# Kernel tuning notes

Hardware: AMD Instinct MI355X
Metric: run time of the kernel (lower is better)

Reference implementation:

```python
import jax, jax.numpy as jnp
import numpy as np

K_NN = 20  # neighbors per group (k=20 in source)


def fps_one(xyz, npoint):
    # xyz: [N,3] -> indices [npoint] via iterative furthest point sampling
    N = xyz.shape[0]
    def body(carry, _):
        dist, far = carry
        d = jnp.sum((xyz - xyz[far]) ** 2, axis=-1)
        dist = jnp.minimum(dist, d)
        return (dist, jnp.argmax(dist).astype(jnp.int32)), far
    init = (jnp.full((N,), 1e10, xyz.dtype), jnp.int32(0))
    _, idx = jax.lax.scan(body, init, None, length=npoint)
    return idx


def gather(pts, idx):
    # pts: [B,M,C], idx: [B,...] -> [B,...,C]
    return jax.vmap(lambda p, i: p[i])(pts, idx)


def knn(q, ref, k):
    # q: [B,S,3], ref: [B,M,3] -> [B,S,k] indices of nearest refs
    d = (jnp.sum(q * q, -1, keepdims=True)
         - 2.0 * jnp.einsum('bsc,bmc->bsm', q, ref)
         + jnp.sum(ref * ref, -1)[:, None, :])
    _, idx = jax.lax.top_k(-d, k)
    return idx


def sa_block(xyz, feats, npoint, W, b):
    # Set abstraction: FPS sample -> kNN group -> shared MLP -> max pool
    fidx = jax.vmap(fps_one, in_axes=(0, None))(xyz, npoint)   # [B,S]
    new_xyz = gather(xyz, fidx)                                 # [B,S,3]
    nidx = knn(new_xyz, xyz, K_NN)                              # [B,S,K]
    rel = gather(xyz, nidx) - new_xyz[:, :, None, :]            # [B,S,K,3]
    grp = jnp.concatenate([rel, gather(feats, nidx)], -1)       # [B,S,K,3+C]
    h = jax.nn.relu(jnp.einsum('bskc,cd->bskd', grp, W) + b)
    return new_xyz, jnp.max(h, axis=2)                          # [B,S,Cout]


def fp_block(xq, xr, fr, skip, W, b):
    # Feature propagation: 3-NN inverse-distance interp -> concat skip -> MLP
    idx = knn(xq, xr, 3)                                        # [B,S,3]
    d = jnp.sum((gather(xr, idx) - xq[:, :, None, :]) ** 2, -1)
    w = 1.0 / (d + 1e-8)
    w = w / jnp.sum(w, -1, keepdims=True)
    interp = jnp.einsum('bsk,bskc->bsc', w, gather(fr, idx))
    cat = jnp.concatenate([interp, skip], -1)
    return jax.nn.relu(jnp.einsum('bsc,cd->bsd', cat, W) + b)


def setup_inputs() -> dict:
    key = jax.random.key(0)
    ks = jax.random.split(key, 24)
    B, N = 8, 4096
    x = jax.random.normal(ks[0], (B, 6, N), jnp.float32)
    cls_label = jax.random.uniform(ks[1], (B, 16), jnp.float32)
    def lin(k, cin, cout):
        kw, kb = jax.random.split(k)
        s = 1.0 / np.sqrt(cin)
        return (jax.random.normal(kw, (cin, cout), jnp.float32) * s,
                jax.random.normal(kb, (cout,), jnp.float32) * 0.01)
    W0, b0 = lin(ks[2], 6, 64)
    W1, b1 = lin(ks[3], 67, 128)
    W2, b2 = lin(ks[4], 131, 256)
    W3, b3 = lin(ks[5], 259, 512)
    F3, fb3 = lin(ks[6], 768, 512)
    F2, fb2 = lin(ks[7], 640, 256)
    F1, fb1 = lin(ks[8], 320, 128)
    F0, fb0 = lin(ks[9], 150, 128)
    Wseg, bseg = lin(ks[10], 128, 50)
    return {"x": x, "cls_label": cls_label,
            "W0": W0, "b0": b0, "W1": W1, "b1": b1, "W2": W2, "b2": b2,
            "W3": W3, "b3": b3, "F3": F3, "fb3": fb3, "F2": F2, "fb2": fb2,
            "F1": F1, "fb1": fb1, "F0": F0, "fb0": fb0,
            "Wseg": Wseg, "bseg": bseg}


def reference(x, cls_label, W0, b0, W1, b1, W2, b2, W3, b3,
              F3, fb3, F2, fb2, F1, fb1, F0, fb0, Wseg, bseg):
    B, _, N = x.shape
    xyz = jnp.transpose(x[:, :3, :], (0, 2, 1))   # [B,N,3]
    nrm = jnp.transpose(x[:, 3:, :], (0, 2, 1))   # [B,N,3]
    # hierarchical set abstraction (512 -> 256 -> 128 -> 64 points)
    x1, f1 = sa_block(xyz, nrm, 512, W0, b0)      # f1: [B,512,64]
    x2, f2 = sa_block(x1, f1, 256, W1, b1)        # f2: [B,256,128]
    x3, f3 = sa_block(x2, f2, 128, W2, b2)        # f3: [B,128,256]
    x4, f4 = sa_block(x3, f3, 64, W3, b3)         # f4: [B,64,512]
    # feature propagation back up
    g3 = fp_block(x3, x4, f4, f3, F3, fb3)        # [B,128,512]
    g2 = fp_block(x2, x3, g3, f2, F2, fb2)        # [B,256,256]
    g1 = fp_block(x1, x2, g2, f1, F1, fb1)        # [B,512,128]
    cls = jnp.broadcast_to(cls_label[:, None, :], (B, N, 16))
    skip0 = jnp.concatenate([cls, xyz, nrm], -1)  # [B,N,22]
    g0 = fp_block(xyz, x1, g1, skip0, F0, fb0)    # [B,N,128]
    result = jnp.einsum('bnc,cd->bnd', g0, Wseg) + bseg  # [B,N,50]
    return result, jnp.transpose(g0, (0, 2, 1))
```

## Files before the change

kernel.cpp:

```cpp
#include <hip/hip_runtime.h>
#include <float.h>

#define B8 8
#define NPTS 4096

template <int CTRL, int RM>
__device__ __forceinline__ unsigned dppmov(unsigned v) {
  return (unsigned)__builtin_amdgcn_update_dpp((int)v, (int)v, CTRL, RM, 0xf, false);
}

template <int CTRL, int RM>
__device__ __forceinline__ void red_key_max(unsigned& kh, unsigned& kl) {
  unsigned oh = dppmov<CTRL, RM>(kh);
  unsigned ol = dppmov<CTRL, RM>(kl);
  unsigned long long ko = ((unsigned long long)oh << 32) | ol;
  unsigned long long k  = ((unsigned long long)kh << 32) | kl;
  bool c = ko > k;
  kh = c ? oh : kh;
  kl = c ? ol : kl;
}

template <int CTRL, int RM>
__device__ __forceinline__ void red_key_min(unsigned& kh, unsigned& kl) {
  unsigned oh = dppmov<CTRL, RM>(kh);
  unsigned ol = dppmov<CTRL, RM>(kl);
  unsigned long long ko = ((unsigned long long)oh << 32) | ol;
  unsigned long long k  = ((unsigned long long)kh << 32) | kl;
  bool c = ko < k;
  kh = c ? oh : kh;
  kl = c ? ol : kl;
}

#define WAVE_RED_MAX(kh, kl)            \
  red_key_max<0x111, 0xf>(kh, kl);      \
  red_key_max<0x112, 0xf>(kh, kl);      \
  red_key_max<0x114, 0xf>(kh, kl);      \
  red_key_max<0x118, 0xf>(kh, kl);      \
  red_key_max<0x142, 0xa>(kh, kl);      \
  red_key_max<0x143, 0xc>(kh, kl);

#define WAVE_RED_MIN(kh, kl)            \
  red_key_min<0x111, 0xf>(kh, kl);      \
  red_key_min<0x112, 0xf>(kh, kl);      \
  red_key_min<0x114, 0xf>(kh, kl);      \
  red_key_min<0x118, 0xf>(kh, kl);      \
  red_key_min<0x142, 0xa>(kh, kl);      \
  red_key_min<0x143, 0xc>(kh, kl);

template <int BLOCK, int P>
__global__ __launch_bounds__(BLOCK) void fps4_kernel(const float* __restrict__ x,
                                                     float* __restrict__ xyz,
                                                     float* __restrict__ nrm,
                                                     float4* __restrict__ xyz4,
                                                     int N, int S,
                                                     float* __restrict__ out_xyz) {
#pragma clang fp contract(off)
  constexpr int NW = BLOCK / 64;
  __shared__ float4 pts[BLOCK * P];
  __shared__ float4 sel[512];
  __shared__ alignas(16) unsigned long long wkey[2][NW];
  int b = blockIdx.x, t = threadIdx.x;
  const float* xb = x + (size_t)b * 6 * N;
  float px[P], py[P], pz[P], dist[P];
#pragma unroll
  for (int j = 0; j < P; ++j) {
    int idx = t + j * BLOCK;
    float a = xb[0 * N + idx], bb = xb[1 * N + idx], c = xb[2 * N + idx];
    px[j] = a; py[j] = bb; pz[j] = c;
    pts[idx] = make_float4(a, bb, c, 0.f);
    dist[j] = 1e10f;
    size_t g = (size_t)b * N + idx;
    float* o1 = xyz + g * 3;
    o1[0] = a; o1[1] = bb; o1[2] = c;
    xyz4[g] = make_float4(a, bb, c, a * a + bb * bb + c * c);
    float n0 = xb[3 * N + idx], n1 = xb[4 * N + idx], n2 = xb[5 * N + idx];
    float* o2 = nrm + g * 3;
    o2[0] = n0; o2[1] = n1; o2[2] = n2;
  }
  __syncthreads();
  float fx = xb[0], fy = xb[N], fz = xb[2 * N];
  for (int i = 0; i < S; ++i) {
    if (t == 0) sel[i] = make_float4(fx, fy, fz, 0.f);
    float bv = -1.0f;
    int bj = 0;
#pragma unroll
    for (int j = 0; j < P; ++j) {
      float dx = px[j] - fx, dy = py[j] - fy, dz = pz[j] - fz;
      float d = dx * dx + dy * dy + dz * dz;
      float nd = fminf(dist[j], d);
      dist[j] = nd;
      bool c = nd > bv;
      bv = c ? nd : bv;
      bj = c ? j : bj;
    }
    unsigned kh = __float_as_uint(bv);
    unsigned kl = (unsigned)(~(t + bj * BLOCK));
    WAVE_RED_MAX(kh, kl);
    int buf = i & 1;
    if ((t & 63) == 63)
      wkey[buf][t >> 6] = ((unsigned long long)kh << 32) | kl;
    __syncthreads();
    unsigned long long g = 0ull;
    const ulonglong2* wk2 = (const ulonglong2*)&wkey[buf][0];
#pragma unroll
    for (int w = 0; w < NW / 2; ++w) {
      ulonglong2 e = wk2[w];
      unsigned long long m = (e.x > e.y) ? e.x : e.y;
      g = (m > g) ? m : g;
    }
    int far = (int)~(unsigned)g;
    float4 f = pts[far];
    fx = f.x; fy = f.y; fz = f.z;
  }
  __syncthreads();
  for (int i = t; i < S; i += BLOCK) {
    float4 f = sel[i];
    float* o = out_xyz + ((size_t)b * S + i) * 3;
    o[0] = f.x; o[1] = f.y; o[2] = f.z;
  }
}

__global__ __launch_bounds__(64) void knn20_kernel(const float* __restrict__ q,
                                                   const float4* __restrict__ ref4,
                                                   const float* __restrict__ nrm,
                                                   const float* __restrict__ W,
                                                   const float* __restrict__ bias,
                                                   float* __restrict__ f1) {
#pragma clang fp contract(off)
  int bs = blockIdx.x;
  int b = bs >> 9;
  int t = threadIdx.x;
  __shared__ alignas(16) float smem_in[20][8];
  const float* qp = q + (size_t)bs * 3;
  float qx = qp[0], qy = qp[1], qz = qp[2];
  float qq = qx * qx + qy * qy + qz * qz;
  const float4* rp = ref4 + (size_t)b * 4096;
  float v1 = FLT_MAX, v2 = FLT_MAX;
  int i1 = 0, i2 = 0;
  for (int k = 0; k < 64; ++k) {
    int i = t + (k << 6);
    float4 r = rp[i];
    float dot = qx * r.x + qy * r.y + qz * r.z;
    float d = qq - 2.0f * dot + r.w;
    if (d < v1) { v2 = v1; i2 = i1; v1 = d; i1 = i; }
    else if (d < v2) { v2 = d; i2 = i; }
  }
  unsigned long long taken = 0ull;
  unsigned keep = 0;
  for (int k = 0; k < 20; ++k) {
    unsigned kh = __float_as_uint(v1), kl = (unsigned)i1;
    WAVE_RED_MIN(kh, kl);
    unsigned w = (unsigned)__builtin_amdgcn_readlane((int)kl, 63);
    if (t == k) keep = w;
    if (((int)w & 63) == t) {
      taken |= 1ull << ((int)w >> 6);
      v1 = v2; i1 = i2;
      v2 = FLT_MAX; i2 = 0;
      if (v1 == FLT_MAX) {
        for (int j = 0; j < 64; ++j) {
          if ((taken >> j) & 1ull) continue;
          int i = t + (j << 6);
          float4 r = rp[i];
          float dot = qx * r.x + qy * r.y + qz * r.z;
          float d = qq - 2.0f * dot + r.w;
          if (d < v1) { v2 = v1; i2 = i1; v1 = d; i1 = i; }
          else if (d < v2) { v2 = d; i2 = i; }
        }
      }
    }
  }
  if (t < 20) {
    int id = (int)keep;
    float4 r = rp[id];
    const float* nr = nrm + ((size_t)b * 4096 + id) * 3;
    smem_in[t][0] = r.x - qx;
    smem_in[t][1] = r.y - qy;
    smem_in[t][2] = r.z - qz;
    smem_in[t][3] = nr[0];
    smem_in[t][4] = nr[1];
    smem_in[t][5] = nr[2];
    smem_in[t][6] = 0.0f;
    smem_in[t][7] = 0.0f;
  }
  __syncthreads();
  float w0 = W[0 * 64 + t], w1 = W[1 * 64 + t], w2 = W[2 * 64 + t];
  float w3 = W[3 * 64 + t], w4 = W[4 * 64 + t], w5 = W[5 * 64 + t];
  float bb = bias[t];
  float m = 0.0f;
  for (int n = 0; n < 20; ++n) {
    const float4 a = *reinterpret_cast<const float4*>(&smem_in[n][0]);
    const float4 c = *reinterpret_cast<const float4*>(&smem_in[n][4]);
    float v = a.x * w0;
    v += a.y * w1;
    v += a.z * w2;
    v += a.w * w3;
    v += c.x * w4;
    v += c.y * w5;
    v += bb;
    m = fmaxf(m, v);
  }
  f1[(size_t)bs * 64 + t] = m;
}

__device__ __forceinline__ void knn3_store(int g, const float* rx3,
                                           float qx, float qy, float qz,
                                           int i0, int i1, int i2,
                                           int* __restrict__ idx3,
                                           float* __restrict__ w3) {
#pragma clang fp contract(off)
  int ii[3] = {i0, i1, i2};
  float w[3];
  float wsum = 0.0f;
#pragma unroll
  for (int k = 0; k < 3; ++k) {
    const float* r = rx3 + (size_t)ii[k] * 3;
    float dx = r[0] - qx, dy = r[1] - qy, dz = r[2] - qz;
    float d = dx * dx + dy * dy + dz * dz;
    w[k] = 1.0f / (d + 1e-8f);
    wsum += w[k];
  }
#pragma unroll
  for (int k = 0; k < 3; ++k) {
    idx3[(size_t)g * 3 + k] = ii[k];
    w3[(size_t)g * 3 + k] = w[k] / wsum;
  }
}

__global__ __launch_bounds__(256) void neighbors_kernel(
    const float* __restrict__ xyz, const float* __restrict__ x1,
    int* __restrict__ nidx2, int* __restrict__ nidx3, int* __restrict__ nidx4,
    int* __restrict__ idx3_3, float* __restrict__ w3_3,
    int* __restrict__ idx3_2, float* __restrict__ w3_2,
    int* __restrict__ idx3_1, float* __restrict__ w3_1,
    int* __restrict__ idx3_0, float* __restrict__ w3_0) {
#pragma clang fp contract(off)
  __shared__ float4 smem4[512];
  int blk = blockIdx.x, tid = threadIdx.x;

  if (blk < 896) {
    int S, M, qid;
    int* nout;
    const int wv = tid >> 6, t64 = tid & 63;
    if (blk < 512)      { S = 256; M = 512; qid = blk * 4 + wv;         nout = nidx2; }
    else if (blk < 768) { S = 128; M = 256; qid = (blk - 512) * 4 + wv; nout = nidx3; }
    else                { S = 64;  M = 128; qid = (blk - 768) * 4 + wv; nout = nidx4; }
    float* swd = (float*)smem4 + wv * M;
    int b = qid / S, s = qid % S;
    const float* qp = x1 + ((size_t)b * 512 + s) * 3;
    float qx = qp[0], qy = qp[1], qz = qp[2];
    float qq = qx * qx + qy * qy + qz * qz;
    const float* rp = x1 + (size_t)b * 512 * 3;
    for (int i = t64; i < M; i += 64) {
      float rx = rp[3 * i], ry = rp[3 * i + 1], rz = rp[3 * i + 2];
      float rr = rx * rx + ry * ry + rz * rz;
      float dot = qx * rx + qy * ry + qz * rz;
      swd[i] = qq - 2.0f * dot + rr;
    }
    __syncthreads();
    unsigned keep = 0;
    for (int k = 0; k < 20; ++k) {
      float bv = FLT_MAX;
      int bi = 0;
      for (int i = t64; i < M; i += 64) {
        float v = swd[i];
        bool c = v < bv;
        bv = c ? v : bv;
        bi = c ? i : bi;
      }
      unsigned kh = __float_as_uint(bv), kl = (unsigned)bi;
      WAVE_RED_MIN(kh, kl);
      unsigned w = (unsigned)__builtin_amdgcn_readlane((int)kl, 63);
      if (t64 == k) keep = w;
      if (t64 == 0) swd[w] = FLT_MAX;
      __syncthreads();
    }
    if (t64 < 20) nout[(size_t)qid * 20 + t64] = (int)keep;
    return;
  }

  if (blk < 900) {
    int g = (blk - 896) * 256 + tid;
    int Sq = 128, M = 64;
    int b = g / Sq, s = g % Sq;
    const float* qp = x1 + ((size_t)b * 512 + s) * 3;
    float qx = qp[0], qy = qp[1], qz = qp[2];
    float qq = qx * qx + qy * qy + qz * qz;
    const float* rp = x1 + (size_t)b * 512 * 3;
    float v0 = FLT_MAX, v1 = FLT_MAX, v2 = FLT_MAX;
    int i0 = 0, i1 = 0, i2 = 0;
    for (int i = 0; i < M; ++i) {
      float rx = rp[3 * i], ry = rp[3 * i + 1], rz = rp[3 * i + 2];
      float d = qq - 2.0f * (qx * rx + qy * ry + qz * rz) + (rx * rx + ry * ry + rz * rz);
      if (d < v2) {
        if (d < v1) {
          if (d < v0) { v2 = v1; i2 = i1; v1 = v0; i1 = i0; v0 = d; i0 = i; }
          else { v2 = v1; i2 = i1; v1 = d; i1 = i; }
        } else { v2 = d; i2 = i; }
      }
    }
    knn3_store(g, rp, qx, qy, qz, i0, i1, i2, idx3_3, w3_3);
    return;
  }

  int g, Sq, M, LDQ;
  int* oidx;
  float* ow;
  const float* q;
  if (blk < 908)      { g = (blk - 900) * 256 + tid; Sq = 256;  M = 128; oidx = idx3_2; ow = w3_2; q = x1;  LDQ = 512; }
  else if (blk < 924) { g = (blk - 908) * 256 + tid; Sq = 512;  M = 256; oidx = idx3_1; ow = w3_1; q = x1;  LDQ = 512; }
  else                { g = (blk - 924) * 256 + tid; Sq = 4096; M = 512; oidx = idx3_0; ow = w3_0; q = xyz; LDQ = 4096; }
  int b = g / Sq, s = g % Sq;
  const float* rp = x1 + (size_t)b * 512 * 3;
  for (int i = tid; i < M; i += 256) {
    float rx = rp[3 * i], ry = rp[3 * i + 1], rz = rp[3 * i + 2];
    smem4[i] = make_float4(rx, ry, rz, rx * rx + ry * ry + rz * rz);
  }
  __syncthreads();
  const float* qp = q + ((size_t)b * LDQ + s) * 3;
  float qx = qp[0], qy = qp[1], qz = qp[2];
  float qq = qx * qx + qy * qy + qz * qz;
  float v0 = FLT_MAX, v1 = FLT_MAX, v2 = FLT_MAX;
  int i0 = 0, i1 = 0, i2 = 0;
  for (int i = 0; i < M; ++i) {
    float4 r = smem4[i];
    float d = qq - 2.0f * (qx * r.x + qy * r.y + qz * r.z) + r.w;
    if (d < v2) {
      if (d < v1) {
        if (d < v0) { v2 = v1; i2 = i1; v1 = v0; i1 = i0; v0 = d; i0 = i; }
        else { v2 = v1; i2 = i1; v1 = d; i1 = i; }
      } else { v2 = d; i2 = i; }
    }
  }
  {
    int ii[3] = {i0, i1, i2};
    float w[3];
    float wsum = 0.0f;
#pragma unroll
    for (int k = 0; k < 3; ++k) {
      float4 r = smem4[ii[k]];
      float dx = r.x - qx, dy = r.y - qy, dz = r.z - qz;
      float d = dx * dx + dy * dy + dz * dz;
      w[k] = 1.0f / (d + 1e-8f);
      wsum += w[k];
    }
#pragma unroll
    for (int k = 0; k < 3; ++k) {
      oidx[(size_t)g * 3 + k] = ii[k];
      ow[(size_t)g * 3 + k] = w[k] / wsum;
    }
  }
}

#define GEMM_SHARED                                                               \
  __shared__ alignas(16) float As[2][16][68];                                     \
  __shared__ alignas(16) float Bs[2][16][64];

#define GEMM_STAGE(k0v, ...)                                                      \
    {                                                                             \
      int kq0 = (k0v) + (((int)threadIdx.x >> 6) << 2);                           \
      float4 va = make_float4(0.f, 0.f, 0.f, 0.f);                                \
      { __VA_ARGS__ }                                                             \
      areg4 = va;                                                                 \
    }                                                                             \
    {                                                                             \
      int kk = (int)threadIdx.x >> 4;                                             \
      int n4 = ((int)threadIdx.x & 15) * 4;                                       \
      int kq = (k0v) + kk, cc = colBase + n4;                                     \
      if (colBase + 64 <= N) {                                                    \
        if (kq < K) breg4 = *reinterpret_cast<const float4*>(&Wm[(size_t)kq * N + cc]); \
        else breg4 = make_float4(0.f, 0.f, 0.f, 0.f);                             \
      } else {                                                                    \
        breg4.x = (kq < K && cc < N) ? Wm[(size_t)kq * N + cc] : 0.0f;            \
        breg4.y = (kq < K && cc + 1 < N) ? Wm[(size_t)kq * N + cc + 1] : 0.0f;    \
        breg4.z = (kq < K && cc + 2 < N) ? Wm[(size_t)kq * N + cc + 2] : 0.0f;    \
        breg4.w = (kq < K && cc + 3 < N) ? Wm[(size_t)kq * N + cc + 3] : 0.0f;    \
      }                                                                           \
    }

#define GEMM_WRITE_LDS(bufv)                                                      \
    {                                                                             \
      int r_ = (int)threadIdx.x & 63;                                             \
      int k4_ = ((int)threadIdx.x >> 6) * 4;                                      \
      As[bufv][k4_ + 0][r_] = areg4.x;                                            \
      As[bufv][k4_ + 1][r_] = areg4.y;                                            \
      As[bufv][k4_ + 2][r_] = areg4.z;                                            \
      As[bufv][k4_ + 3][r_] = areg4.w;                                            \
    }                                                                             \
    *reinterpret_cast<float4*>(&Bs[bufv][threadIdx.x >> 4][(threadIdx.x & 15) * 4]) = breg4;

#define GEMM_MAIN(...)                                                            \
  int tx = threadIdx.x & 15, ty = threadIdx.x >> 4;                               \
  float acc[4][4] = {};                                                           \
  float4 areg4, breg4;                                                            \
  GEMM_STAGE(kLo, __VA_ARGS__)                                                    \
  GEMM_WRITE_LDS(0)                                                               \
  __syncthreads();                                                                \
  int cur = 0;                                                                    \
  for (int k0 = kLo; k0 < kHi; k0 += 16) {                                        \
    int nxt = cur ^ 1;                                                            \
    bool more = (k0 + 16 < kHi);                                                  \
    if (more) { GEMM_STAGE(k0 + 16, __VA_ARGS__) }                                \
    _Pragma("unroll")                                                             \
    for (int kk = 0; kk < 16; ++kk) {                                             \
      const float4 av = *reinterpret_cast<const float4*>(&As[cur][kk][ty * 4]);   \
      const float4 bv = *reinterpret_cast<const float4*>(&Bs[cur][kk][tx * 4]);   \
      acc[0][0] += av.x * bv.x; acc[0][1] += av.x * bv.y;                         \
      acc[0][2] += av.x * bv.z; acc[0][3] += av.x * bv.w;                         \
      acc[1][0] += av.y * bv.x; acc[1][1] += av.y * bv.y;                         \
      acc[1][2] += av.y * bv.z; acc[1][3] += av.y * bv.w;                         \
      acc[2][0] += av.z * bv.x; acc[2][1] += av.z * bv.y;                         \
      acc[2][2] += av.z * bv.z; acc[2][3] += av.z * bv.w;                         \
      acc[3][0] += av.w * bv.x; acc[3][1] += av.w * bv.y;                         \
      acc[3][2] += av.w * bv.z; acc[3][3] += av.w * bv.w;                         \
    }                                                                             \
    if (more) { GEMM_WRITE_LDS(nxt) }                                             \
    __syncthreads();                                                              \
    cur = nxt;                                                                    \
  }

#define GEMM_EPI_STORE                                                            \
  _Pragma("unroll")                                                               \
  for (int i = 0; i < 4; ++i) {                                                   \
    int row = rowBase + ty * 4 + i;                                               \
    if (row >= Mrows) continue;                                                   \
    _Pragma("unroll")                                                             \
    for (int j = 0; j < 4; ++j) {                                                 \
      int col = colBase + tx * 4 + j;                                             \
      if (col >= N) continue;                                                     \
      float v = acc[i][j] + bias[col];                                            \
      if (RELU) v = fmaxf(v, 0.0f);                                               \
      C[(size_t)row * N + col] = v;                                               \
    }                                                                             \
  }

__global__ __launch_bounds__(256) void gemm_seg_kernel(const float* __restrict__ A,
                                                       const float* __restrict__ Wm,
                                                       const float* __restrict__ bias,
                                                       float* __restrict__ C,
                                                       float* __restrict__ T,
                                                       int Mrows, int N, int K) {
  GEMM_SHARED
  const int kLo = 0, kHi = K;
  const int RELU = 0;
  int rowBase = blockIdx.y * 64;
  int colBase = blockIdx.x * 64;
  const int rowA = rowBase + ((int)threadIdx.x & 63);
  const float* arow = A + (size_t)rowA * K;
  float* tbase = T + ((size_t)(rowA >> 12) * 128) * 4096 + (rowA & 4095);
  GEMM_MAIN(
    va = *reinterpret_cast<const float4*>(&arow[kq0]);
    {
      float* tp = tbase + (size_t)kq0 * 4096;
      tp[0] = va.x; tp[4096] = va.y; tp[8192] = va.z; tp[12288] = va.w;
    }
  )
  GEMM_EPI_STORE
}

__global__ __launch_bounds__(256) void gemm_sa_kernel(
    const float* __restrict__ xyz, const float* __restrict__ feats,
    const float* __restrict__ new_xyz, const int* __restrict__ nidx,
    const float* __restrict__ Wm, const float* __restrict__ bias,
    float* __restrict__ fOut, int Mref, int LDR, int S, int LDQ, int Cf,
    int Mrows, int N, int K) {
  GEMM_SHARED
  const int kLo = 0, kHi = K;
  int rowBase = blockIdx.y * 64;
  int colBase = blockIdx.x * 64;
  const int rowA = rowBase + ((int)threadIdx.x & 63);
  const int bsA = rowA / 20;
  const int sA = bsA % S;
  const int bA = bsA / S;
  const int idA = nidx[rowA];
  const float* xrA = xyz + ((size_t)bA * LDR + idA) * 3;
  const float* xqA = new_xyz + ((size_t)bA * LDQ + sA) * 3;
  const float* fbA = feats + ((size_t)bA * Mref + idA) * Cf;
  GEMM_MAIN(
    float* vp_ = (float*)&va;
    _Pragma("unroll")
    for (int c_ = 0; c_ < 4; ++c_) {
      int kq = kq0 + c_;
      float v = 0.0f;
      if (kq < K) v = (kq < 3) ? (xrA[kq] - xqA[kq]) : fbA[kq - 3];
      vp_[c_] = v;
    }
  )
  __shared__ int smax[4][64];
  int gBase = rowBase / 20;
  int nG = (rowBase + 63) / 20 - gBase + 1;
  for (int l = threadIdx.x; l < nG * 64; l += 256) smax[l >> 6][l & 63] = 0;
  __syncthreads();
  {
    int gl = (rowBase + ty * 4) / 20 - gBase;
#pragma unroll
    for (int j = 0; j < 4; ++j) {
      int col = colBase + tx * 4 + j;
      if (col >= N) continue;
      float bb = bias[col];
      float m = 0.0f;
#pragma unroll
      for (int i = 0; i < 4; ++i) {
        int row = rowBase + ty * 4 + i;
        if (row >= Mrows) continue;
        m = fmaxf(m, fmaxf(acc[i][j] + bb, 0.0f));
      }
      atomicMax(&smax[gl][tx * 4 + j], __float_as_int(m));
    }
  }
  __syncthreads();
  for (int l = threadIdx.x; l < nG * 64; l += 256) {
    int g = gBase + (l >> 6), c = colBase + (l & 63);
    if (c < N) atomicMax((int*)&fOut[(size_t)g * N + c], smax[l >> 6][l & 63]);
  }
}

__global__ __launch_bounds__(256) void gemm_fp_kernel(
    const float* __restrict__ fr, const int* __restrict__ idx3,
    const float* __restrict__ w3, const float* __restrict__ skip,
    const float* __restrict__ cls, const float* __restrict__ xyzq,
    const float* __restrict__ nrmq, const float* __restrict__ frBias,
    const float* __restrict__ Wm, const float* __restrict__ bias,
    float* __restrict__ C, int Sq, int Mr, int Cr, int Cs, int mode,
    int SPLITK, int CHUNK,
    int Mrows, int N, int K) {
  GEMM_SHARED
  const int kLo = blockIdx.z * CHUNK;
  const int kHi = min(K, kLo + CHUNK);
  int rowBase = blockIdx.y * 64;
  int colBase = blockIdx.x * 64;
  const int rowA = rowBase + ((int)threadIdx.x & 63);
  const int bA = rowA / Sq;
  const int* iiA = idx3 + (size_t)rowA * 3;
  const float* wwA = w3 + (size_t)rowA * 3;
  const float* fbA = fr + (size_t)bA * Mr * Cr;
  const float* f0A = fbA + (size_t)iiA[0] * Cr;
  const float* f1A = fbA + (size_t)iiA[1] * Cr;
  const float* f2A = fbA + (size_t)iiA[2] * Cr;
  const float w0A = wwA[0], w1A = wwA[1], w2A = wwA[2];
  const float* skipA = skip ? skip + (size_t)rowA * Cs : nullptr;
  const float* clsA = cls ? cls + (size_t)bA * 16 : nullptr;
  const float* xyzqA = xyzq ? xyzq + (size_t)rowA * 3 : nullptr;
  const float* nrmqA = nrmq ? nrmq + (size_t)rowA * 3 : nullptr;
  GEMM_MAIN(
    float* vp_ = (float*)&va;
    _Pragma("unroll")
    for (int c_ = 0; c_ < 4; ++c_) {
      int kq = kq0 + c_;
      float v = 0.0f;
      if (kq < K) {
        if (kq < Cr) {
          float a0 = f0A[kq];
          float a1 = f1A[kq];
          float a2 = f2A[kq];
          if (frBias) {
            float bb = frBias[kq];
            a0 = fmaxf(a0 + bb, 0.0f);
            a1 = fmaxf(a1 + bb, 0.0f);
            a2 = fmaxf(a2 + bb, 0.0f);
          }
          v = w0A * a0;
          v += w1A * a1;
          v += w2A * a2;
        } else {
          int cc = kq - Cr;
          if (mode == 0) {
            v = skipA[cc];
          } else {
            if (cc < 16) v = clsA[cc];
            else if (cc < 19) v = xyzqA[cc - 16];
            else v = nrmqA[cc - 19];
          }
        }
      }
      vp_[c_] = v;
    }
  )
  if (SPLITK) {
#pragma unroll
    for (int i = 0; i < 4; ++i) {
      int row = rowBase + ty * 4 + i;
      if (row >= Mrows) continue;
#pragma unroll
      for (int j = 0; j < 4; ++j) {
        int col = colBase + tx * 4 + j;
        if (col >= N) continue;
        atomicAdd(&C[(size_t)row * N + col], acc[i][j]);
      }
    }
  } else {
    const int RELU = 1;
    GEMM_EPI_STORE
  }
}

static inline int cdiv(int a, int b) { return (a + b - 1) / b; }

extern "C" void kernel_launch(void* const* d_in, const int* in_sizes, int n_in,
                              void* d_out, int out_size, void* d_ws, size_t ws_size,
                              hipStream_t stream) {
  const float* x    = (const float*)d_in[0];
  const float* cls  = (const float*)d_in[1];
  const float* W0 = (const float*)d_in[2];  const float* b0 = (const float*)d_in[3];
  const float* W1 = (const float*)d_in[4];  const float* b1 = (const float*)d_in[5];
  const float* W2 = (const float*)d_in[6];  const float* b2 = (const float*)d_in[7];
  const float* W3 = (const float*)d_in[8];  const float* b3 = (const float*)d_in[9];
  const float* F3 = (const float*)d_in[10]; const float* fb3 = (const float*)d_in[11];
  const float* F2 = (const float*)d_in[12]; const float* fb2 = (const float*)d_in[13];
  const float* F1 = (const float*)d_in[14]; const float* fb1 = (const float*)d_in[15];
  const float* F0 = (const float*)d_in[16]; const float* fb0 = (const float*)d_in[17];
  const float* Wseg = (const float*)d_in[18]; const float* bseg = (const float*)d_in[19];
  float* out = (float*)d_out;

  float* ws = (float*)d_ws;
  size_t off = 0;
  auto alloc = [&](size_t n) { float* p = ws + off; off += (n + 3) & ~(size_t)3; return p; };
  float* xyz = alloc(8 * 4096 * 3);
  float* nrm = alloc(8 * 4096 * 3);
  float4* xyz4 = (float4*)alloc(8 * 4096 * 4);
  float* x1 = alloc(8 * 512 * 3);
  float* f1 = alloc(8 * 512 * 64);
  float* f2 = alloc(8 * 256 * 128);
  float* f3 = alloc(8 * 128 * 256);
  float* f4 = alloc(8 * 64 * 512);
  float* g3 = alloc(8 * 128 * 512);
  float* g2 = alloc(8 * 256 * 256);
  float* g1 = alloc(8 * 512 * 128);
  float* g0 = alloc(8 * 4096 * 128);
  int* nidx2 = (int*)alloc(8 * 256 * 20);
  int* nidx3 = (int*)alloc(8 * 128 * 20);
  int* nidx4 = (int*)alloc(8 * 64 * 20);
  int* idx3_3 = (int*)alloc(8 * 128 * 3);  float* w3_3 = alloc(8 * 128 * 3);
  int* idx3_2 = (int*)alloc(8 * 256 * 3);  float* w3_2 = alloc(8 * 256 * 3);
  int* idx3_1 = (int*)alloc(8 * 512 * 3);  float* w3_1 = alloc(8 * 512 * 3);
  int* idx3_0 = (int*)alloc(8 * 4096 * 3); float* w3_0 = alloc(8 * 4096 * 3);

  hipMemsetAsync(f1, 0,
                 ((size_t)8 * (512 * 64 + 256 * 128 + 128 * 256 + 64 * 512) +
                  (size_t)8 * (128 * 512 + 256 * 256 + 512 * 128)) * 4, stream);

  fps4_kernel<256, 16><<<8, 256, 0, stream>>>(x, xyz, nrm, xyz4, 4096, 512, x1);
  knn20_kernel<<<8 * 512, 64, 0, stream>>>(x1, xyz4, nrm, W0, b0, f1);
  neighbors_kernel<<<1052, 256, 0, stream>>>(xyz, x1, nidx2, nidx3, nidx4,
                                             idx3_3, w3_3, idx3_2, w3_2,
                                             idx3_1, w3_1, idx3_0, w3_0);

  {
    dim3 grid(2, cdiv(8 * 256 * 20, 64));
    gemm_sa_kernel<<<grid, 256, 0, stream>>>(x1, f1, x1, nidx2, W1, b1, f2,
                                             512, 512, 256, 512, 64,
                                             8 * 256 * 20, 128, 67);
  }
  {
    dim3 grid(4, cdiv(8 * 128 * 20, 64));
    gemm_sa_kernel<<<grid, 256, 0, stream>>>(x1, f2, x1, nidx3, W2, b2, f3,
                                             256, 512, 128, 512, 128,
                                             8 * 128 * 20, 256, 131);
  }
  {
    dim3 grid(8, cdiv(8 * 64 * 20, 64));
    gemm_sa_kernel<<<grid, 256, 0, stream>>>(x1, f3, x1, nidx4, W3, b3, f4,
                                             128, 512, 64, 512, 256,
                                             8 * 64 * 20, 512, 259);
  }

  {
    dim3 grid(8, cdiv(8 * 128, 64), 4);
    gemm_fp_kernel<<<grid, 256, 0, stream>>>(f4, idx3_3, w3_3, f3, nullptr, nullptr, nullptr,
                                             nullptr, F3, fb3, g3, 128, 64, 512, 256, 0,
                                             1, 192, 8 * 128, 512, 768);
  }
  {
    dim3 grid(4, cdiv(8 * 256, 64), 4);
    gemm_fp_kernel<<<grid, 256, 0, stream>>>(g3, idx3_2, w3_2, f2, nullptr, nullptr, nullptr,
                                             fb3, F2, fb2, g2, 256, 128, 512, 128, 0,
                                             1, 160, 8 * 256, 256, 640);
  }
  {
    dim3 grid(2, cdiv(8 * 512, 64), 2);
    gemm_fp_kernel<<<grid, 256, 0, stream>>>(g2, idx3_1, w3_1, f1, nullptr, nullptr, nullptr,
                                             fb2, F1, fb1, g1, 512, 256, 256, 64, 0,
                                             1, 160, 8 * 512, 128, 320);
  }
  {
    dim3 grid(2, cdiv(8 * 4096, 64), 1);
    gemm_fp_kernel<<<grid, 256, 0, stream>>>(g1, idx3_0, w3_0, nullptr, cls, xyz, nrm,
                                             fb1, F0, fb0, g0, 4096, 512, 128, 22, 1,
                                             0, 160, 8 * 4096, 128, 150);
  }

  {
    dim3 grid(1, cdiv(8 * 4096, 64));
    gemm_seg_kernel<<<grid, 256, 0, stream>>>(g0, Wseg, bseg, out,
                                              out + (size_t)8 * 4096 * 50,
                                              8 * 4096, 50, 128);
  }
}
```

Measured before the change: 958.1 us.

## Split FP interpolation into separate kernel and feed dense float4 GEMM

Moves the 3-NN inverse-distance interpolation and skip concatenation out of the GEMM A-tile loader into a standalone interp_kernel that writes a dense A matrix to a workspace buffer. The GEMM then loads A with float4 vector loads instead of three gathered scalar loads plus bias/relu per element, which were repeated for every column block. This adds extra kernel launches and a global round-trip through the new buffer. The memset is also narrowed to skip f1.

```diff
diff --git a/kernel.cpp b/kernel.cpp
--- a/kernel.cpp
+++ b/kernel.cpp
@@ -348,6 +348,42 @@
       oidx[(size_t)g * 3 + k] = ii[k];
       ow[(size_t)g * 3 + k] = w[k] / wsum;
     }
+  }
+}
+
+__global__ __launch_bounds__(256) void interp_kernel(
+    const float* __restrict__ fr, const int* __restrict__ idx3,
+    const float* __restrict__ w3, const float* __restrict__ skip,
+    const float* __restrict__ frBias,
+    float* __restrict__ A, int Sq, int Mr, int Cr, int Cs, int LDA) {
+#pragma clang fp contract(off)
+  int row = blockIdx.x * 4 + ((int)threadIdx.x >> 6);
+  int t = (int)threadIdx.x & 63;
+  int b = row / Sq;
+  const int* ii = idx3 + (size_t)row * 3;
+  const float* ww = w3 + (size_t)row * 3;
+  const float* fb = fr + (size_t)b * Mr * Cr;
+  const float* f0 = fb + (size_t)ii[0] * Cr;
+  const float* f1 = fb + (size_t)ii[1] * Cr;
+  const float* f2 = fb + (size_t)ii[2] * Cr;
+  float w0 = ww[0], w1 = ww[1], w2 = ww[2];
+  float* arow = A + (size_t)row * LDA;
+  for (int kq = t; kq < Cr; kq += 64) {
+    float a0 = f0[kq], a1 = f1[kq], a2 = f2[kq];
+    if (frBias) {
+      float bb = frBias[kq];
+      a0 = fmaxf(a0 + bb, 0.0f);
+      a1 = fmaxf(a1 + bb, 0.0f);
+      a2 = fmaxf(a2 + bb, 0.0f);
+    }
+    float v = w0 * a0;
+    v += w1 * a1;
+    v += w2 * a2;
+    arow[kq] = v;
+  }
+  if (skip) {
+    const float* sk = skip + (size_t)row * Cs;
+    for (int kq = t; kq < Cs; kq += 64) arow[Cr + kq] = sk[kq];
   }
 }
 
@@ -514,65 +550,43 @@
   }
 }
 
-__global__ __launch_bounds__(256) void gemm_fp_kernel(
-    const float* __restrict__ fr, const int* __restrict__ idx3,
-    const float* __restrict__ w3, const float* __restrict__ skip,
+__global__ __launch_bounds__(256) void gemm_dense_kernel(
+    const float* __restrict__ A, int LDA, int KA,
     const float* __restrict__ cls, const float* __restrict__ xyzq,
-    const float* __restrict__ nrmq, const float* __restrict__ frBias,
+    const float* __restrict__ nrmq,
     const float* __restrict__ Wm, const float* __restrict__ bias,
-    float* __restrict__ C, int Sq, int Mr, int Cr, int Cs, int mode,
-    int SPLITK, int CHUNK,
-    int Mrows, int N, int K) {
+    float* __restrict__ C, int Mrows, int N, int K,
+    int RELU, int SPLITK, int CHUNK, int Sq) {
   GEMM_SHARED
   const int kLo = blockIdx.z * CHUNK;
   const int kHi = min(K, kLo + CHUNK);
   int rowBase = blockIdx.y * 64;
   int colBase = blockIdx.x * 64;
   const int rowA = rowBase + ((int)threadIdx.x & 63);
-  const int bA = rowA / Sq;
-  const int* iiA = idx3 + (size_t)rowA * 3;
-  const float* wwA = w3 + (size_t)rowA * 3;
-  const float* fbA = fr + (size_t)bA * Mr * Cr;
-  const float* f0A = fbA + (size_t)iiA[0] * Cr;
-  const float* f1A = fbA + (size_t)iiA[1] * Cr;
-  const float* f2A = fbA + (size_t)iiA[2] * Cr;
-  const float w0A = wwA[0], w1A = wwA[1], w2A = wwA[2];
-  const float* skipA = skip ? skip + (size_t)rowA * Cs : nullptr;
+  const float* arow = A + (size_t)rowA * LDA;
+  const int bA = Sq ? rowA / Sq : 0;
   const float* clsA = cls ? cls + (size_t)bA * 16 : nullptr;
   const float* xyzqA = xyzq ? xyzq + (size_t)rowA * 3 : nullptr;
   const float* nrmqA = nrmq ? nrmq + (size_t)rowA * 3 : nullptr;
   GEMM_MAIN(
-    float* vp_ = (float*)&va;
-    _Pragma("unroll")
-    for (int c_ = 0; c_ < 4; ++c_) {
-      int kq = kq0 + c_;
-      float v = 0.0f;
-      if (kq < K) {
-        if (kq < Cr) {
-          float a0 = f0A[kq];
-          float a1 = f1A[kq];
-          float a2 = f2A[kq];
-          if (frBias) {
-            float bb = frBias[kq];
-            a0 = fmaxf(a0 + bb, 0.0f);
-            a1 = fmaxf(a1 + bb, 0.0f);
-            a2 = fmaxf(a2 + bb, 0.0f);
-          }
-          v = w0A * a0;
-          v += w1A * a1;
-          v += w2A * a2;
-        } else {
-          int cc = kq - Cr;
-          if (mode == 0) {
-            v = skipA[cc];
-          } else {
-            if (cc < 16) v = clsA[cc];
-            else if (cc < 19) v = xyzqA[cc - 16];
-            else v = nrmqA[cc - 19];
-          }
+    if (kq0 + 3 < KA) {
+      va = *reinterpret_cast<const float4*>(&arow[kq0]);
+    } else {
+      float* vp_ = (float*)&va;
+      _Pragma("unroll")
+      for (int c_ = 0; c_ < 4; ++c_) {
+        int kq = kq0 + c_;
+        float v = 0.0f;
+        if (kq < KA) {
+          v = arow[kq];
+        } else if (kq < K) {
+          int cc = kq - KA;
+          if (cc < 16) v = clsA[cc];
+          else if (cc < 19) v = xyzqA[cc - 16];
+          else v = nrmqA[cc - 19];
         }
+        vp_[c_] = v;
       }
-      vp_[c_] = v;
     }
   )
   if (SPLITK) {
@@ -588,7 +602,6 @@
       }
     }
   } else {
-    const int RELU = 1;
     GEMM_EPI_STORE
   }
 }
@@ -626,6 +639,7 @@
   float* g2 = alloc(8 * 256 * 256);
   float* g1 = alloc(8 * 512 * 128);
   float* g0 = alloc(8 * 4096 * 128);
+  float* Abuf = alloc((size_t)8 * 4096 * 128);
   int* nidx2 = (int*)alloc(8 * 256 * 20);
   int* nidx3 = (int*)alloc(8 * 128 * 20);
   int* nidx4 = (int*)alloc(8 * 64 * 20);
@@ -634,8 +648,8 @@
   int* idx3_1 = (int*)alloc(8 * 512 * 3);  float* w3_1 = alloc(8 * 512 * 3);
   int* idx3_0 = (int*)alloc(8 * 4096 * 3); float* w3_0 = alloc(8 * 4096 * 3);
 
-  hipMemsetAsync(f1, 0,
-                 ((size_t)8 * (512 * 64 + 256 * 128 + 128 * 256 + 64 * 512) +
+  hipMemsetAsync(f2, 0,
+                 ((size_t)8 * (256 * 128 + 128 * 256 + 64 * 512) +
                   (size_t)8 * (128 * 512 + 256 * 256 + 512 * 128)) * 4, stream);
 
   fps4_kernel<256, 16><<<8, 256, 0, stream>>>(x, xyz, nrm, xyz4, 4096, 512, x1);
@@ -663,29 +677,41 @@
                                              8 * 64 * 20, 512, 259);
   }
 
+  interp_kernel<<<8 * 128 / 4, 256, 0, stream>>>(f4, idx3_3, w3_3, f3, nullptr,
+                                                 Abuf, 128, 64, 512, 256, 768);
   {
     dim3 grid(8, cdiv(8 * 128, 64), 4);
-    gemm_fp_kernel<<<grid, 256, 0, stream>>>(f4, idx3_3, w3_3, f3, nullptr, nullptr, nullptr,
-                                             nullptr, F3, fb3, g3, 128, 64, 512, 256, 0,
-                                             1, 192, 8 * 128, 512, 768);
-  }
+    gemm_dense_kernel<<<grid, 256, 0, stream>>>(Abuf, 768, 768,
+                                                nullptr, nullptr, nullptr,
+                                                F3, fb3, g3, 8 * 128, 512, 768,
+                                                0, 1, 192, 0);
+  }
+  interp_kernel<<<8 * 256 / 4, 256, 0, stream>>>(g3, idx3_2, w3_2, f2, fb3,
+                                                 Abuf, 256, 128, 512, 128, 640);
   {
     dim3 grid(4, cdiv(8 * 256, 64), 4);
-    gemm_fp_kernel<<<grid, 256, 0, stream>>>(g3, idx3_2, w3_2, f2, nullptr, nullptr, nullptr,
-                                             fb3, F2, fb2, g2, 256, 128, 512, 128, 0,
-                                             1, 160, 8 * 256, 256, 640);
-  }
+    gemm_dense_kernel<<<grid, 256, 0, stream>>>(Abuf, 640, 640,
+                                                nullptr, nullptr, nullptr,
+                                                F2, fb2, g2, 8 * 256, 256, 640,
+                                                0, 1, 160, 0);
+  }
+  interp_kernel<<<8 * 512 / 4, 256, 0, stream>>>(g2, idx3_1, w3_1, f1, fb2,
+                                                 Abuf, 512, 256, 256, 64, 320);
   {
     dim3 grid(2, cdiv(8 * 512, 64), 2);
-    gemm_fp_kernel<<<grid, 256, 0, stream>>>(g2, idx3_1, w3_1, f1, nullptr, nullptr, nullptr,
-                                             fb2, F1, fb1, g1, 512, 256, 256, 64, 0,
-                                             1, 160, 8 * 512, 128, 320);
-  }
+    gemm_dense_kernel<<<grid, 256, 0, stream>>>(Abuf, 320, 320,
+                                                nullptr, nullptr, nullptr,
+                                                F1, fb1, g1, 8 * 512, 128, 320,
+                                                0, 1, 160, 0);
+  }
+  interp_kernel<<<8 * 4096 / 4, 256, 0, stream>>>(g1, idx3_0, w3_0, nullptr, fb1,
+                                                  Abuf, 4096, 512, 128, 0, 128);
   {
     dim3 grid(2, cdiv(8 * 4096, 64), 1);
-    gemm_fp_kernel<<<grid, 256, 0, stream>>>(g1, idx3_0, w3_0, nullptr, cls, xyz, nrm,
-                                             fb1, F0, fb0, g0, 4096, 512, 128, 22, 1,
-                                             0, 160, 8 * 4096, 128, 150);
+    gemm_dense_kernel<<<grid, 256, 0, stream>>>(Abuf, 128, 128,
+                                                cls, xyz, nrm,
+                                                F0, fb0, g0, 8 * 4096, 128, 150,
+                                                1, 0, 160, 4096);
   }
 
   {
```

After: 912.6 us. 4.7% less time.
